# Optimization experiments

Measured on AMD Instinct MI355X. Metric: run time of the kernel, lower is better.

## Reference

```python
import jax, jax.numpy as jnp
import numpy as np

V, E, H, L, T, B = 50257, 1024, 16, 12, 128, 16
FF = 4 * E
STD = 0.02


def setup_inputs() -> dict:
    key = jax.random.key(0)
    ks = jax.random.split(key, 20)
    n = lambda k, shape: (jax.random.normal(k, shape, dtype=jnp.float32) * STD)
    inp = {
        'idx': jax.random.randint(ks[0], (B, T), 0, V, dtype=jnp.int64),
        'targets': jax.random.randint(ks[1], (B, T), 0, V, dtype=jnp.int64),
        'tok_emb': n(ks[2], (V, E)),
        'pos_emb': n(ks[3], (T, E)),
        'wq': n(ks[4], (L, E, E)),
        'wk': n(ks[5], (L, E, E)),
        'wv': n(ks[6], (L, E, E)),
        'w_proj': n(ks[7], (L, E, E)),
        'b_proj': jnp.zeros((L, E), jnp.float32),
        'ln1_g': jnp.ones((L, E), jnp.float32),
        'ln1_b': jnp.zeros((L, E), jnp.float32),
        'ln2_g': jnp.ones((L, E), jnp.float32),
        'ln2_b': jnp.zeros((L, E), jnp.float32),
        'w_fc1': n(ks[8], (L, E, FF)),
        'b_fc1': jnp.zeros((L, FF), jnp.float32),
        'w_fc2': n(ks[9], (L, FF, E)),
        'b_fc2': jnp.zeros((L, E), jnp.float32),
        'lnf_g': jnp.ones((E,), jnp.float32),
        'lnf_b': jnp.zeros((E,), jnp.float32),
        'w_head': n(ks[10], (E, V)),
        'b_head': jnp.zeros((V,), jnp.float32),
    }
    return inp


def _layernorm(x, g, b, eps=1e-5):
    m = x.mean(-1, keepdims=True)
    v = ((x - m) ** 2).mean(-1, keepdims=True)
    return (x - m) / jnp.sqrt(v + eps) * g + b


def _forward(idx, targets, tok_emb, pos_emb, wq, wk, wv, w_proj, b_proj,
             ln1_g, ln1_b, ln2_g, ln2_b, w_fc1, b_fc1, w_fc2, b_fc2,
             lnf_g, lnf_b, w_head, b_head):
    Bb, Tt = idx.shape
    x = tok_emb[idx] + pos_emb[:Tt]  # (B, T, E)
    causal = jnp.tril(jnp.ones((Tt, Tt), dtype=bool))
    scale = E ** (-0.5)  # NOTE: original scales by full n_embd, not head_size

    def block(x, p):
        (wq_l, wk_l, wv_l, wp_l, bp_l, g1, b1, g2, b2, wf1, bf1, wf2, bf2) = p
        h = _layernorm(x, g1, b1)
        q = (h @ wq_l).reshape(Bb, Tt, H, -1)
        k = (h @ wk_l).reshape(Bb, Tt, H, -1)
        v = (h @ wv_l).reshape(Bb, Tt, H, -1)
        sc = jnp.einsum('bthd,bshd->bhts', q, k) * scale
        sc = jnp.where(causal, sc, -jnp.inf)
        att = jax.nn.softmax(sc, axis=-1)
        o = jnp.einsum('bhts,bshd->bthd', att, v).reshape(Bb, Tt, E)
        x = x + o @ wp_l + bp_l
        h2 = _layernorm(x, g2, b2)
        x = x + jax.nn.relu(h2 @ wf1 + bf1) @ wf2 + bf2
        return x, None

    x, _ = jax.lax.scan(block, x, (wq, wk, wv, w_proj, b_proj, ln1_g, ln1_b,
                                   ln2_g, ln2_b, w_fc1, b_fc1, w_fc2, b_fc2))
    x = _layernorm(x, lnf_g, lnf_b)
    logits = x @ w_head + b_head  # (B, T, V)
    logp = jax.nn.log_softmax(logits, axis=-1)
    nll = -jnp.take_along_axis(logp.reshape(Bb * Tt, -1),
                               targets.reshape(-1, 1), axis=1)
    loss = nll.mean()
    return logits, loss


def reference(idx, targets, tok_emb, pos_emb, wq, wk, wv, w_proj, b_proj,
              ln1_g, ln1_b, ln2_g, ln2_b, w_fc1, b_fc1, w_fc2, b_fc2,
              lnf_g, lnf_b, w_head, b_head):
    return _forward(idx, targets, tok_emb, pos_emb, wq, wk, wv, w_proj, b_proj,
                    ln1_g, ln1_b, ln2_g, ln2_b, w_fc1, b_fc1, w_fc2, b_fc2,
                    lnf_g, lnf_b, w_head, b_head)
```

## Files before the change

### kernel.cpp

```cpp
#include <hip/hip_runtime.h>
#include <math.h>

typedef unsigned short u16;
typedef float f32x4 __attribute__((ext_vector_type(4)));
typedef short bf16x8 __attribute__((ext_vector_type(8)));
typedef unsigned short us4 __attribute__((ext_vector_type(4)));

#define DEVI __device__ __forceinline__

DEVI float bf2f(u16 u) { return __uint_as_float(((unsigned int)u) << 16); }
DEVI u16 f2bf(float f) {
    unsigned int u = __float_as_uint(f);
    u += 0x7fffu + ((u >> 16) & 1u);
    return (u16)(u >> 16);
}

__global__ __launch_bounds__(256) void k_embed(const int* __restrict__ idx,
                                               const float* __restrict__ te,
                                               const float* __restrict__ pe,
                                               float* __restrict__ x) {
    int m = blockIdx.x;
    int t = m & 127;
    int tok = idx[m];
    const f32x4* a = (const f32x4*)(te + (long)tok * 1024);
    const f32x4* p = (const f32x4*)(pe + (long)t * 1024);
    f32x4* o = (f32x4*)(x + (long)m * 1024);
    o[threadIdx.x] = a[threadIdx.x] + p[threadIdx.x];
}

__global__ __launch_bounds__(256) void k_ln(const float* __restrict__ x,
                                            const float* __restrict__ g,
                                            const float* __restrict__ b,
                                            u16* __restrict__ out) {
    __shared__ float red[8];
    int tid = threadIdx.x, lane = tid & 63, wid = tid >> 6;
    int r = blockIdx.x;
    f32x4 v = ((const f32x4*)(x + (long)r * 1024))[tid];
    float s = v.x + v.y + v.z + v.w;
#pragma unroll
    for (int o2 = 32; o2; o2 >>= 1) s += __shfl_xor(s, o2);
    if (lane == 0) red[wid] = s;
    __syncthreads();
    float mean = (red[0] + red[1] + red[2] + red[3]) * (1.0f / 1024.0f);
    f32x4 d; d.x = v.x - mean; d.y = v.y - mean; d.z = v.z - mean; d.w = v.w - mean;
    float sq = d.x * d.x + d.y * d.y + d.z * d.z + d.w * d.w;
#pragma unroll
    for (int o2 = 32; o2; o2 >>= 1) sq += __shfl_xor(sq, o2);
    if (lane == 0) red[4 + wid] = sq;
    __syncthreads();
    float rstd = rsqrtf((red[4] + red[5] + red[6] + red[7]) * (1.0f / 1024.0f) + 1e-5f);
    f32x4 gg = ((const f32x4*)g)[tid];
    f32x4 bb = ((const f32x4*)b)[tid];
    us4 o4;
    o4.x = f2bf(d.x * rstd * gg.x + bb.x);
    o4.y = f2bf(d.y * rstd * gg.y + bb.y);
    o4.z = f2bf(d.z * rstd * gg.z + bb.z);
    o4.w = f2bf(d.w * rstd * gg.w + bb.w);
    ((us4*)(out + (long)r * 1024))[tid] = o4;
}

DEVI void tr_tile(const float* __restrict__ in, u16* __restrict__ out,
                  int K, int N, int k0, int n0, int tid, float (*tile)[65]) {
    int trow = tid >> 4;
    int tcol = (tid & 15) * 4;
#pragma unroll
    for (int p = 0; p < 4; ++p) {
        int k = k0 + trow + p * 16;
        const float* src = in + (long)k * N + n0 + tcol;
#pragma unroll
        for (int j = 0; j < 4; ++j) {
            int n = n0 + tcol + j;
            tile[trow + p * 16][tcol + j] = (n < N) ? src[j] : 0.0f;
        }
    }
    __syncthreads();
#pragma unroll
    for (int p = 0; p < 4; ++p) {
        int n = n0 + trow + p * 16;
        if (n < N) {
            us4 o4;
#pragma unroll
            for (int j = 0; j < 4; ++j) o4[j] = f2bf(tile[tcol + j][trow + p * 16]);
            *(us4*)(out + (long)n * K + k0 + tcol) = o4;
        }
    }
}

__global__ __launch_bounds__(256) void k_tr_one(const float* __restrict__ in,
                                                u16* __restrict__ out, int K, int N) {
    __shared__ float tile[64][65];
    tr_tile(in, out, K, N, blockIdx.y * 64, blockIdx.x * 64, threadIdx.x, tile);
}

__global__ __launch_bounds__(256) void k_tr_layer(
    const float* __restrict__ wq, const float* __restrict__ wk,
    const float* __restrict__ wv, const float* __restrict__ wp,
    const float* __restrict__ f1, const float* __restrict__ f2,
    u16* __restrict__ oqkv, u16* __restrict__ oproj,
    u16* __restrict__ of1, u16* __restrict__ of2) {
    __shared__ float tile[64][65];
    int id = blockIdx.x;
    const float* in; u16* out; int K, N, txx, tyy;
    if (id < 1024) {
        int t = id >> 8, s2 = id & 255;
        txx = s2 & 15; tyy = s2 >> 4; K = 1024; N = 1024;
        in = (t == 0) ? wq : (t == 1) ? wk : (t == 2) ? wv : wp;
        out = (t == 3) ? oproj : oqkv + (long)t * 1024 * 1024;
    } else if (id < 2048) {
        int s2 = id - 1024;
        txx = s2 & 63; tyy = s2 >> 6; K = 1024; N = 4096; in = f1; out = of1;
    } else {
        int s2 = id - 2048;
        txx = s2 & 15; tyy = s2 >> 4; K = 4096; N = 1024; in = f2; out = of2;
    }
    tr_tile(in, out, K, N, tyy * 64, txx * 64, threadIdx.x, tile);
}

template <int ROWS>
DEVI void stage_tile(const u16* __restrict__ g, long row0, long rowmax, int ld,
                     int col0, char* lds, int tid) {
    constexpr int NCH = ROWS * 8;
#pragma unroll
    for (int p = 0; p < NCH / 256; ++p) {
        int c = tid + p * 256;
        int row = c >> 3;
        int gslot = c & 7;
        int gdata = gslot ^ (row & 7);
        long gr = row0 + row;
        if (gr > rowmax) gr = rowmax;
        const u16* src = g + gr * (long)ld + col0 + gdata * 8;
        char* dst = lds + ((long)((tid & 192) + p * 256)) * 16;
        __builtin_amdgcn_global_load_lds(
            (const __attribute__((address_space(1))) void*)src,
            (__attribute__((address_space(3))) void*)dst, 16, 0, 0);
    }
}

template <int ROWS>
DEVI void stage512(const u16* __restrict__ g, long row0, long rowmax, int ld,
                   int col0, char* lds, int tid) {
    constexpr int NP = ROWS * 8 / 512;
#pragma unroll
    for (int p = 0; p < NP; ++p) {
        int c = tid + p * 512;
        int row = c >> 3;
        int gslot = c & 7;
        int gdata = gslot ^ (row & 7);
        long gr = row0 + row;
        if (gr > rowmax) gr = rowmax;
        const u16* src = g + gr * (long)ld + col0 + gdata * 8;
        char* dst = lds + ((long)((tid & 448) + p * 512)) * 16;
        __builtin_amdgcn_global_load_lds(
            (const __attribute__((address_space(1))) void*)src,
            (__attribute__((address_space(3))) void*)dst, 16, 0, 0);
    }
}

template <int BN, bool OUT_BF16, bool RELU, bool HAS_BIAS, bool HAS_RES>
__global__ __launch_bounds__(256, 2) void k_gemm(
    const u16* __restrict__ A, const u16* __restrict__ Bt,
    const float* __restrict__ bias, const float* __restrict__ res,
    float* __restrict__ Cf, u16* __restrict__ Cb,
    int M, int N, int K, int ldc) {
    constexpr int NR = BN / 32;
    constexpr int ASZ = 128 * 64 * 2;
    constexpr int BSZ = BN * 64 * 2;
    __shared__ __align__(16) char lds[2 * (ASZ + BSZ)];
    int tid = threadIdx.x, lane = tid & 63, wid = tid >> 6;
    int l15 = lane & 15, l4 = lane >> 4;
    int wr = wid >> 1, wc = wid & 1;
    long m0 = (long)blockIdx.y * 128;
    long n0 = (long)blockIdx.x * BN;
    f32x4 acc[4][NR] = {};
    const int nk = K >> 6;

    stage_tile<128>(A, m0, (long)M - 1, K, 0, lds, tid);
    stage_tile<BN>(Bt, n0, (long)N - 1, K, 0, lds + ASZ, tid);
    int cur = 0;
    for (int kt = 0; kt < nk; ++kt) {
        __syncthreads();
        if (kt + 1 < nk) {
            char* nb = lds + (cur ^ 1) * (ASZ + BSZ);
            stage_tile<128>(A, m0, (long)M - 1, K, (kt + 1) << 6, nb, tid);
            stage_tile<BN>(Bt, n0, (long)N - 1, K, (kt + 1) << 6, nb + ASZ, tid);
        }
        const char* ab = lds + cur * (ASZ + BSZ);
        const char* bb = ab + ASZ;
#pragma unroll
        for (int kh = 0; kh < 2; ++kh) {
            bf16x8 af[4], bfv[NR];
#pragma unroll
            for (int mi = 0; mi < 4; ++mi) {
                int row = wr * 64 + mi * 16 + l15;
                int slot = (kh * 4 + l4) ^ (row & 7);
                af[mi] = *(const bf16x8*)(ab + (row * 8 + slot) * 16);
            }
#pragma unroll
            for (int ni = 0; ni < NR; ++ni) {
                int row = wc * (BN / 2) + ni * 16 + l15;
                int slot = (kh * 4 + l4) ^ (row & 7);
                bfv[ni] = *(const bf16x8*)(bb + (row * 8 + slot) * 16);
            }
#pragma unroll
            for (int mi = 0; mi < 4; ++mi)
#pragma unroll
                for (int ni = 0; ni < NR; ++ni)
                    acc[mi][ni] = __builtin_amdgcn_mfma_f32_16x16x32_bf16(
                        af[mi], bfv[ni], acc[mi][ni], 0, 0, 0);
        }
        cur ^= 1;
    }
#pragma unroll
    for (int ni = 0; ni < NR; ++ni) {
        long n = n0 + wc * (BN / 2) + ni * 16 + l15;
        if (n < N) {
            float bv = HAS_BIAS ? bias[n] : 0.0f;
#pragma unroll
            for (int mi = 0; mi < 4; ++mi) {
#pragma unroll
                for (int j = 0; j < 4; ++j) {
                    long m = m0 + wr * 64 + mi * 16 + l4 * 4 + j;
                    float v = acc[mi][ni][j] + bv;
                    if (HAS_RES) v += res[m * (long)ldc + n];
                    if (RELU) v = fmaxf(v, 0.0f);
                    if (OUT_BF16) Cb[m * (long)ldc + n] = f2bf(v);
                    else Cf[m * (long)ldc + n] = v;
                }
            }
        }
    }
}

__global__ __launch_bounds__(512, 1) void k_head256(
    const u16* __restrict__ A, const u16* __restrict__ Bt,
    const float* __restrict__ bias, float* __restrict__ Cf,
    float2* __restrict__ part, int M, int N, int K, int ldc) {
    constexpr int ASZ = 256 * 64 * 2;
    constexpr int BSZ = 128 * 64 * 2;
    __shared__ __align__(16) char lds[256 * 129 * 4];
    int tid = threadIdx.x, lane = tid & 63, wid = tid >> 6;
    int l15 = lane & 15, l4 = lane >> 4;
    int wr = wid >> 1, wc = wid & 1;
    int bn = blockIdx.x, bm = blockIdx.y;
    long m0 = (long)bm * 256, n0 = (long)bn * 128;
    f32x4 acc[4][4] = {};
    const int nk = K >> 6;

    stage512<256>(A, m0, (long)M - 1, K, 0, lds, tid);
    stage512<128>(Bt, n0, (long)N - 1, K, 0, lds + ASZ, tid);
    int cur = 0;
    for (int kt = 0; kt < nk; ++kt) {
        __syncthreads();
        if (kt + 1 < nk) {
            char* nb = lds + (cur ^ 1) * (ASZ + BSZ);
            stage512<256>(A, m0, (long)M - 1, K, (kt + 1) << 6, nb, tid);
            stage512<128>(Bt, n0, (long)N - 1, K, (kt + 1) << 6, nb + ASZ, tid);
        }
        const char* ab = lds + cur * (ASZ + BSZ);
        const char* bb = ab + ASZ;
#pragma unroll
        for (int kh = 0; kh < 2; ++kh) {
            bf16x8 af[4], bfv[4];
#pragma unroll
            for (int mi = 0; mi < 4; ++mi) {
                int row = wr * 64 + mi * 16 + l15;
                int slot = (kh * 4 + l4) ^ (row & 7);
                af[mi] = *(const bf16x8*)(ab + (row * 8 + slot) * 16);
            }
#pragma unroll
            for (int ni = 0; ni < 4; ++ni) {
                int row = wc * 64 + ni * 16 + l15;
                int slot = (kh * 4 + l4) ^ (row & 7);
                bfv[ni] = *(const bf16x8*)(bb + (row * 8 + slot) * 16);
            }
#pragma unroll
            for (int mi = 0; mi < 4; ++mi)
#pragma unroll
                for (int ni = 0; ni < 4; ++ni)
                    acc[mi][ni] = __builtin_amdgcn_mfma_f32_16x16x32_bf16(
                        af[mi], bfv[ni], acc[mi][ni], 0, 0, 0);
        }
        cur ^= 1;
    }
    const float BIG_NEG = -1e30f;
    float bvv[4];
#pragma unroll
    for (int ni = 0; ni < 4; ++ni) {
        long n = n0 + wc * 64 + ni * 16 + l15;
        bvv[ni] = (n < N) ? bias[n] : 0.0f;
    }
    __syncthreads();
    float* ldsF = (float*)lds;
#pragma unroll
    for (int mi = 0; mi < 4; ++mi)
#pragma unroll
        for (int ni = 0; ni < 4; ++ni)
#pragma unroll
            for (int j = 0; j < 4; ++j) {
                int row = wr * 64 + mi * 16 + l4 * 4 + j;
                int col = wc * 64 + ni * 16 + l15;
                long n = n0 + col;
                float v = acc[mi][ni][j] + bvv[ni];
                if (n >= N) v = BIG_NEG;
                ldsF[row * 129 + col] = v;
            }
    __syncthreads();
#pragma unroll 4
    for (int i = 0; i < 64; ++i) {
        int flat = tid + (i << 9);
        int row = flat >> 7, col = flat & 127;
        long n = n0 + col;
        if (n < N)
            __builtin_nontemporal_store(ldsF[row * 129 + col],
                                        &Cf[(m0 + row) * (long)ldc + n]);
    }
    {
        int r = tid >> 1, half = tid & 1;
        const float* rp = ldsF + r * 129 + half * 64;
        float mx = BIG_NEG;
#pragma unroll 8
        for (int c = 0; c < 64; ++c) mx = fmaxf(mx, rp[c]);
        float sm = 0.f;
#pragma unroll 8
        for (int c = 0; c < 64; ++c) sm += __expf(rp[c] - mx);
        float mo = __shfl_xor(mx, 1), so = __shfl_xor(sm, 1);
        float nm = fmaxf(mx, mo);
        float S = sm * __expf(mx - nm) + so * __expf(mo - nm);
        if (half == 0)
            part[(long)bn * M + m0 + r] = make_float2(nm, S);
    }
}

__global__ __launch_bounds__(256) void k_attn_mfma(const u16* __restrict__ qkv,
                                                   u16* __restrict__ o) {
    __shared__ __align__(16) u16 Ks[128 * 64];
    __shared__ __align__(16) u16 Vt[64 * 128];
    __shared__ __align__(16) u16 Ps[4][32 * 128];
    int tid = threadIdx.x, lane = tid & 63, w = tid >> 6;
    int l15 = lane & 15, l4 = lane >> 4;
    int b = blockIdx.x >> 4, h = blockIdx.x & 15;
    const u16* base = qkv + (long)b * 128 * 3072 + h * 64;

    stage_tile<128>(base + 1024, 0, 127, 3072, 0, (char*)Ks, tid);
    {
        const u16* vg = base + 2048;
#pragma unroll
        for (int p = 0; p < 4; ++p) {
            int s0 = (w * 4 + p) * 8;
            u16 tmp[8];
#pragma unroll
            for (int j = 0; j < 8; ++j) tmp[j] = vg[(long)(s0 + j) * 3072 + lane];
            int slot = (s0 >> 3) ^ (lane & 7);
            *(bf16x8*)((char*)Vt + lane * 256 + slot * 16) = *(bf16x8*)tmp;
        }
    }
    bf16x8 aq[2][2];
#pragma unroll
    for (int mj = 0; mj < 2; ++mj)
#pragma unroll
        for (int kk = 0; kk < 2; ++kk)
            aq[mj][kk] = *(const bf16x8*)(base + (long)(w * 32 + mj * 16 + l15) * 3072 + kk * 32 + l4 * 8);
    __syncthreads();

    f32x4 sacc[2][8] = {};
#pragma unroll
    for (int sj = 0; sj < 8; ++sj) {
        bf16x8 bk[2];
#pragma unroll
        for (int kk = 0; kk < 2; ++kk) {
            int row = sj * 16 + l15;
            int slot = (kk * 4 + l4) ^ (row & 7);
            bk[kk] = *(const bf16x8*)((char*)Ks + (row * 8 + slot) * 16);
        }
#pragma unroll
        for (int mj = 0; mj < 2; ++mj) {
            sacc[mj][sj] = __builtin_amdgcn_mfma_f32_16x16x32_bf16(aq[mj][0], bk[0], sacc[mj][sj], 0, 0, 0);
            sacc[mj][sj] = __builtin_amdgcn_mfma_f32_16x16x32_bf16(aq[mj][1], bk[1], sacc[mj][sj], 0, 0, 0);
        }
    }
    const float scale = 0.03125f;
#pragma unroll
    for (int mj = 0; mj < 2; ++mj) {
#pragma unroll
        for (int j = 0; j < 4; ++j) {
            int tq = w * 32 + mj * 16 + l4 * 4 + j;
            float mx = -INFINITY;
#pragma unroll
            for (int sj = 0; sj < 8; ++sj) {
                int s = sj * 16 + l15;
                float v = (s <= tq) ? sacc[mj][sj][j] * scale : -INFINITY;
                sacc[mj][sj][j] = v;
                mx = fmaxf(mx, v);
            }
#pragma unroll
            for (int ofs = 1; ofs < 16; ofs <<= 1) mx = fmaxf(mx, __shfl_xor(mx, ofs));
            float sm = 0.f;
#pragma unroll
            for (int sj = 0; sj < 8; ++sj) {
                float e = __expf(sacc[mj][sj][j] - mx);
                sacc[mj][sj][j] = e;
                sm += e;
            }
#pragma unroll
            for (int ofs = 1; ofs < 16; ofs <<= 1) sm += __shfl_xor(sm, ofs);
            float inv = 1.0f / sm;
            int m2 = mj * 16 + l4 * 4 + j;
            u16* prow = Ps[w] + m2 * 128;
#pragma unroll
            for (int sj = 0; sj < 8; ++sj) {
                int s = sj * 16 + l15;
                int slot = (s >> 3) ^ (m2 & 7);
                prow[slot * 8 + (s & 7)] = f2bf(sacc[mj][sj][j] * inv);
            }
        }
    }
    f32x4 oacc[2][4] = {};
#pragma unroll
    for (int kk = 0; kk < 4; ++kk) {
        bf16x8 pa[2], bv[4];
#pragma unroll
        for (int mj = 0; mj < 2; ++mj) {
            int m2 = mj * 16 + l15;
            int slot = (kk * 4 + l4) ^ (m2 & 7);
            pa[mj] = *(const bf16x8*)((char*)(Ps[w]) + m2 * 256 + slot * 16);
        }
#pragma unroll
        for (int nb = 0; nb < 4; ++nb) {
            int d = nb * 16 + l15;
            int slot = (kk * 4 + l4) ^ (d & 7);
            bv[nb] = *(const bf16x8*)((char*)Vt + d * 256 + slot * 16);
        }
#pragma unroll
        for (int mj = 0; mj < 2; ++mj)
#pragma unroll
            for (int nb = 0; nb < 4; ++nb)
                oacc[mj][nb] = __builtin_amdgcn_mfma_f32_16x16x32_bf16(pa[mj], bv[nb], oacc[mj][nb], 0, 0, 0);
    }
#pragma unroll
    for (int mj = 0; mj < 2; ++mj)
#pragma unroll
        for (int nb = 0; nb < 4; ++nb) {
            int d = nb * 16 + l15;
#pragma unroll
            for (int j = 0; j < 4; ++j) {
                int tq = w * 32 + mj * 16 + l4 * 4 + j;
                o[((long)b * 128 + tq) * 1024 + h * 64 + d] = f2bf(oacc[mj][nb][j]);
            }
        }
}

__global__ __launch_bounds__(64) void k_loss_rows2(const float2* __restrict__ part,
                                                   const float* __restrict__ logits,
                                                   const int* __restrict__ tgt,
                                                   float* __restrict__ rowloss, int ncb) {
    int r = blockIdx.x, lane = threadIdx.x;
    float M = -1e30f, S = 0.f;
    for (int cb = lane; cb < ncb; cb += 64) {
        float2 p = part[(long)cb * 2048 + r];
        float nm = fmaxf(M, p.x);
        S = S * __expf(M - nm) + p.y * __expf(p.x - nm);
        M = nm;
    }
#pragma unroll
    for (int ofs = 32; ofs; ofs >>= 1) {
        float M2 = __shfl_xor(M, ofs), S2 = __shfl_xor(S, ofs);
        float nm = fmaxf(M, M2);
        S = S * __expf(M - nm) + S2 * __expf(M2 - nm);
        M = nm;
    }
    if (lane == 0)
        rowloss[r] = (M + logf(S)) - logits[(long)r * 50257 + tgt[r]];
}

__global__ __launch_bounds__(256) void k_loss_reduce(const float* __restrict__ rowloss,
                                                     float* __restrict__ out) {
    __shared__ float red[4];
    int tid = threadIdx.x, lane = tid & 63, wid = tid >> 6;
    float s = 0.f;
    for (int i = tid; i < 2048; i += 256) s += rowloss[i];
#pragma unroll
    for (int ofs = 32; ofs; ofs >>= 1) s += __shfl_xor(s, ofs);
    if (lane == 0) red[wid] = s;
    __syncthreads();
    if (tid == 0) out[0] = (red[0] + red[1] + red[2] + red[3]) * (1.0f / 2048.0f);
}

extern "C" void kernel_launch(void* const* d_in, const int* in_sizes, int n_in,
                              void* d_out, int out_size, void* d_ws, size_t ws_size,
                              hipStream_t stream) {
    (void)in_sizes; (void)n_in; (void)out_size; (void)ws_size;
    const int*   idx     = (const int*)d_in[0];
    const int*   targets = (const int*)d_in[1];
    const float* tok_emb = (const float*)d_in[2];
    const float* pos_emb = (const float*)d_in[3];
    const float* wq      = (const float*)d_in[4];
    const float* wk      = (const float*)d_in[5];
    const float* wv      = (const float*)d_in[6];
    const float* w_proj  = (const float*)d_in[7];
    const float* b_proj  = (const float*)d_in[8];
    const float* ln1_g   = (const float*)d_in[9];
    const float* ln1_b   = (const float*)d_in[10];
    const float* ln2_g   = (const float*)d_in[11];
    const float* ln2_b   = (const float*)d_in[12];
    const float* w_fc1   = (const float*)d_in[13];
    const float* b_fc1   = (const float*)d_in[14];
    const float* w_fc2   = (const float*)d_in[15];
    const float* b_fc2   = (const float*)d_in[16];
    const float* lnf_g   = (const float*)d_in[17];
    const float* lnf_b   = (const float*)d_in[18];
    const float* w_head  = (const float*)d_in[19];
    const float* b_head  = (const float*)d_in[20];
    float* out = (float*)d_out;

    char* w = (char*)d_ws;
    auto alloc = [&](size_t bytes) {
        char* p = w;
        w += (bytes + 255) & ~(size_t)255;
        return p;
    };
    u16*    wT_qkv  = (u16*)alloc(3072L * 1024 * 2);
    u16*    wT_proj = (u16*)alloc(1024L * 1024 * 2);
    u16*    wT_f1   = (u16*)alloc(4096L * 1024 * 2);
    u16*    wT_f2   = (u16*)alloc(1024L * 4096 * 2);
    u16*    wT_head = (u16*)alloc(50257L * 1024 * 2);
    float*  x       = (float*)alloc(2048L * 1024 * 4);
    u16*    h_bf    = (u16*)alloc(2048L * 1024 * 2);
    u16*    qkvb    = (u16*)alloc(2048L * 3072 * 2);
    u16*    o_bf    = (u16*)alloc(2048L * 1024 * 2);
    u16*    ff_bf   = (u16*)alloc(2048L * 4096 * 2);
    float2* part    = (float2*)alloc(393L * 2048 * 8);
    float*  rowloss = (float*)alloc(2048L * 4);

    k_embed<<<2048, 256, 0, stream>>>(idx, tok_emb, pos_emb, x);
    k_tr_one<<<dim3(786, 16), 256, 0, stream>>>(w_head, wT_head, 1024, 50257);

    for (int l = 0; l < 12; ++l) {
        k_tr_layer<<<3072, 256, 0, stream>>>(
            wq + (long)l * 1048576, wk + (long)l * 1048576,
            wv + (long)l * 1048576, w_proj + (long)l * 1048576,
            w_fc1 + (long)l * 4194304, w_fc2 + (long)l * 4194304,
            wT_qkv, wT_proj, wT_f1, wT_f2);
        k_ln<<<2048, 256, 0, stream>>>(x, ln1_g + l * 1024, ln1_b + l * 1024, h_bf);
        k_gemm<128, true, false, false, false><<<dim3(24, 16), 256, 0, stream>>>(
            h_bf, wT_qkv, nullptr, nullptr, nullptr, qkvb, 2048, 3072, 1024, 3072);
        k_attn_mfma<<<256, 256, 0, stream>>>(qkvb, o_bf);
        k_gemm<64, false, false, true, true><<<dim3(16, 16), 256, 0, stream>>>(
            o_bf, wT_proj, b_proj + l * 1024, x, x, nullptr, 2048, 1024, 1024, 1024);
        k_ln<<<2048, 256, 0, stream>>>(x, ln2_g + l * 1024, ln2_b + l * 1024, h_bf);
        k_gemm<128, true, true, true, false><<<dim3(32, 16), 256, 0, stream>>>(
            h_bf, wT_f1, b_fc1 + l * 4096, nullptr, nullptr, ff_bf, 2048, 4096, 1024, 4096);
        k_gemm<64, false, false, true, true><<<dim3(16, 16), 256, 0, stream>>>(
            ff_bf, wT_f2, b_fc2 + l * 1024, x, x, nullptr, 2048, 1024, 4096, 1024);
    }
    k_ln<<<2048, 256, 0, stream>>>(x, lnf_g, lnf_b, h_bf);
    k_head256<<<dim3(393, 8), 512, 0, stream>>>(h_bf, wT_head, b_head, out, part,
                                                2048, 50257, 1024, 50257);
    k_loss_rows2<<<2048, 64, 0, stream>>>(part, out, targets, rowloss, 393);
    k_loss_reduce<<<1, 256, 0, stream>>>(rowloss, out + 102926336L);
}
```

Baseline: 2.059 ms.

## Triple-buffer LM head GEMM and split-K fc2 with residual folded into LayerNorm

The LM head GEMM moves from a double-buffered loop to a three-stage async LDS pipeline. It uses explicit vmcnt waits and raw barriers, and raises wave priority around the MFMA block. The fc2 GEMM is split into two K halves that write fp32 partial sums to a scratch buffer, which doubles the grid. A new combine+LayerNorm kernel then adds both partials, the bias and the residual, and applies the next LN1 or the final LN in one pass. This buys deeper load overlap and more parallelism, at the cost of extra partial-buffer traffic and more LDS in the head kernel.

Result: faster. 1.913 ms (-7.1%).

```diff
diff --git a/kernel.cpp b/kernel.cpp
--- a/kernel.cpp
+++ b/kernel.cpp
@@ -28,14 +28,8 @@
     o[threadIdx.x] = a[threadIdx.x] + p[threadIdx.x];
 }
 
-__global__ __launch_bounds__(256) void k_ln(const float* __restrict__ x,
-                                            const float* __restrict__ g,
-                                            const float* __restrict__ b,
-                                            u16* __restrict__ out) {
-    __shared__ float red[8];
-    int tid = threadIdx.x, lane = tid & 63, wid = tid >> 6;
-    int r = blockIdx.x;
-    f32x4 v = ((const f32x4*)(x + (long)r * 1024))[tid];
+DEVI void ln_body(f32x4 v, const float* g, const float* b, float* red,
+                  int tid, int lane, int wid, u16* outrow) {
     float s = v.x + v.y + v.z + v.w;
 #pragma unroll
     for (int o2 = 32; o2; o2 >>= 1) s += __shfl_xor(s, o2);
@@ -56,7 +50,37 @@
     o4.y = f2bf(d.y * rstd * gg.y + bb.y);
     o4.z = f2bf(d.z * rstd * gg.z + bb.z);
     o4.w = f2bf(d.w * rstd * gg.w + bb.w);
-    ((us4*)(out + (long)r * 1024))[tid] = o4;
+    ((us4*)outrow)[tid] = o4;
+}
+
+__global__ __launch_bounds__(256) void k_ln(const float* __restrict__ x,
+                                            const float* __restrict__ g,
+                                            const float* __restrict__ b,
+                                            u16* __restrict__ out) {
+    __shared__ float red[8];
+    int tid = threadIdx.x, lane = tid & 63, wid = tid >> 6;
+    int r = blockIdx.x;
+    f32x4 v = ((const f32x4*)(x + (long)r * 1024))[tid];
+    ln_body(v, g, b, red, tid, lane, wid, out + (long)r * 1024);
+}
+
+__global__ __launch_bounds__(256) void k_comb_ln(float* __restrict__ x,
+                                                 const float* __restrict__ p01,
+                                                 const float* __restrict__ bias,
+                                                 const float* __restrict__ g,
+                                                 const float* __restrict__ b,
+                                                 u16* __restrict__ out) {
+    __shared__ float red[8];
+    int tid = threadIdx.x, lane = tid & 63, wid = tid >> 6;
+    int r = blockIdx.x;
+    f32x4 v = ((const f32x4*)(x + (long)r * 1024))[tid];
+    f32x4 p0 = ((const f32x4*)(p01 + (long)r * 1024))[tid];
+    f32x4 p1 = ((const f32x4*)(p01 + 2048L * 1024 + (long)r * 1024))[tid];
+    f32x4 bv = ((const f32x4*)bias)[tid];
+    v.x += p0.x + p1.x + bv.x; v.y += p0.y + p1.y + bv.y;
+    v.z += p0.z + p1.z + bv.z; v.w += p0.w + p1.w + bv.w;
+    ((f32x4*)(x + (long)r * 1024))[tid] = v;
+    ln_body(v, g, b, red, tid, lane, wid, out + (long)r * 1024);
 }
 
 DEVI void tr_tile(const float* __restrict__ in, u16* __restrict__ out,
@@ -156,12 +180,12 @@
     }
 }
 
-template <int BN, bool OUT_BF16, bool RELU, bool HAS_BIAS, bool HAS_RES>
+template <int BN, bool OUT_BF16, bool RELU, bool HAS_BIAS, bool HAS_RES, bool SPLITK>
 __global__ __launch_bounds__(256, 2) void k_gemm(
     const u16* __restrict__ A, const u16* __restrict__ Bt,
     const float* __restrict__ bias, const float* __restrict__ res,
     float* __restrict__ Cf, u16* __restrict__ Cb,
-    int M, int N, int K, int ldc) {
+    int M, int N, int K, int ldk, int ldc) {
     constexpr int NR = BN / 32;
     constexpr int ASZ = 128 * 64 * 2;
     constexpr int BSZ = BN * 64 * 2;
@@ -169,20 +193,26 @@
     int tid = threadIdx.x, lane = tid & 63, wid = tid >> 6;
     int l15 = lane & 15, l4 = lane >> 4;
     int wr = wid >> 1, wc = wid & 1;
+    if constexpr (SPLITK) {
+        int h = blockIdx.z;
+        A += (long)h * K;
+        Bt += (long)h * K;
+        Cf += (long)h * M * (long)ldc;
+    }
     long m0 = (long)blockIdx.y * 128;
     long n0 = (long)blockIdx.x * BN;
     f32x4 acc[4][NR] = {};
     const int nk = K >> 6;
 
-    stage_tile<128>(A, m0, (long)M - 1, K, 0, lds, tid);
-    stage_tile<BN>(Bt, n0, (long)N - 1, K, 0, lds + ASZ, tid);
+    stage_tile<128>(A, m0, (long)M - 1, ldk, 0, lds, tid);
+    stage_tile<BN>(Bt, n0, (long)N - 1, ldk, 0, lds + ASZ, tid);
     int cur = 0;
     for (int kt = 0; kt < nk; ++kt) {
         __syncthreads();
         if (kt + 1 < nk) {
             char* nb = lds + (cur ^ 1) * (ASZ + BSZ);
-            stage_tile<128>(A, m0, (long)M - 1, K, (kt + 1) << 6, nb, tid);
-            stage_tile<BN>(Bt, n0, (long)N - 1, K, (kt + 1) << 6, nb + ASZ, tid);
+            stage_tile<128>(A, m0, (long)M - 1, ldk, (kt + 1) << 6, nb, tid);
+            stage_tile<BN>(Bt, n0, (long)N - 1, ldk, (kt + 1) << 6, nb + ASZ, tid);
         }
         const char* ab = lds + cur * (ASZ + BSZ);
         const char* bb = ab + ASZ;
@@ -237,7 +267,8 @@
     float2* __restrict__ part, int M, int N, int K, int ldc) {
     constexpr int ASZ = 256 * 64 * 2;
     constexpr int BSZ = 128 * 64 * 2;
-    __shared__ __align__(16) char lds[256 * 129 * 4];
+    constexpr int TSZ = ASZ + BSZ;
+    __shared__ __align__(16) char lds[3 * TSZ];
     int tid = threadIdx.x, lane = tid & 63, wid = tid >> 6;
     int l15 = lane & 15, l4 = lane >> 4;
     int wr = wid >> 1, wc = wid & 1;
@@ -246,17 +277,18 @@
     f32x4 acc[4][4] = {};
     const int nk = K >> 6;
 
-    stage512<256>(A, m0, (long)M - 1, K, 0, lds, tid);
-    stage512<128>(Bt, n0, (long)N - 1, K, 0, lds + ASZ, tid);
-    int cur = 0;
-    for (int kt = 0; kt < nk; ++kt) {
-        __syncthreads();
-        if (kt + 1 < nk) {
-            char* nb = lds + (cur ^ 1) * (ASZ + BSZ);
-            stage512<256>(A, m0, (long)M - 1, K, (kt + 1) << 6, nb, tid);
-            stage512<128>(Bt, n0, (long)N - 1, K, (kt + 1) << 6, nb + ASZ, tid);
-        }
-        const char* ab = lds + cur * (ASZ + BSZ);
+#pragma unroll
+    for (int t = 0; t < 3; ++t) {
+        char* buf = lds + t * TSZ;
+        stage512<256>(A, m0, (long)M - 1, K, t << 6, buf, tid);
+        stage512<128>(Bt, n0, (long)N - 1, K, t << 6, buf + ASZ, tid);
+    }
+    for (int t = 0; t < nk; ++t) {
+        if (t + 2 < nk)      asm volatile("s_waitcnt vmcnt(12)" ::: "memory");
+        else if (t + 1 < nk) asm volatile("s_waitcnt vmcnt(6)" ::: "memory");
+        else                 asm volatile("s_waitcnt vmcnt(0)" ::: "memory");
+        __builtin_amdgcn_s_barrier();
+        const char* ab = lds + (t % 3) * TSZ;
         const char* bb = ab + ASZ;
 #pragma unroll
         for (int kh = 0; kh < 2; ++kh) {
@@ -273,14 +305,21 @@
                 int slot = (kh * 4 + l4) ^ (row & 7);
                 bfv[ni] = *(const bf16x8*)(bb + (row * 8 + slot) * 16);
             }
+            __builtin_amdgcn_s_setprio(1);
 #pragma unroll
             for (int mi = 0; mi < 4; ++mi)
 #pragma unroll
                 for (int ni = 0; ni < 4; ++ni)
                     acc[mi][ni] = __builtin_amdgcn_mfma_f32_16x16x32_bf16(
                         af[mi], bfv[ni], acc[mi][ni], 0, 0, 0);
-        }
-        cur ^= 1;
+            __builtin_amdgcn_s_setprio(0);
+        }
+        __builtin_amdgcn_s_barrier();
+        if (t + 3 < nk) {
+            char* buf = lds + (t % 3) * TSZ;
+            stage512<256>(A, m0, (long)M - 1, K, (t + 3) << 6, buf, tid);
+            stage512<128>(Bt, n0, (long)N - 1, K, (t + 3) << 6, buf + ASZ, tid);
+        }
     }
     const float BIG_NEG = -1e30f;
     float bvv[4];
@@ -528,6 +567,7 @@
     u16*    qkvb    = (u16*)alloc(2048L * 3072 * 2);
     u16*    o_bf    = (u16*)alloc(2048L * 1024 * 2);
     u16*    ff_bf   = (u16*)alloc(2048L * 4096 * 2);
+    float*  p01     = (float*)alloc(2L * 2048 * 1024 * 4);
     float2* part    = (float2*)alloc(393L * 2048 * 8);
     float*  rowloss = (float*)alloc(2048L * 4);
 
@@ -540,19 +580,23 @@
             wv + (long)l * 1048576, w_proj + (long)l * 1048576,
             w_fc1 + (long)l * 4194304, w_fc2 + (long)l * 4194304,
             wT_qkv, wT_proj, wT_f1, wT_f2);
-        k_ln<<<2048, 256, 0, stream>>>(x, ln1_g + l * 1024, ln1_b + l * 1024, h_bf);
-        k_gemm<128, true, false, false, false><<<dim3(24, 16), 256, 0, stream>>>(
-            h_bf, wT_qkv, nullptr, nullptr, nullptr, qkvb, 2048, 3072, 1024, 3072);
+        if (l == 0)
+            k_ln<<<2048, 256, 0, stream>>>(x, ln1_g, ln1_b, h_bf);
+        else
+            k_comb_ln<<<2048, 256, 0, stream>>>(x, p01, b_fc2 + (l - 1) * 1024,
+                                                ln1_g + l * 1024, ln1_b + l * 1024, h_bf);
+        k_gemm<128, true, false, false, false, false><<<dim3(24, 16), 256, 0, stream>>>(
+            h_bf, wT_qkv, nullptr, nullptr, nullptr, qkvb, 2048, 3072, 1024, 1024, 3072);
         k_attn_mfma<<<256, 256, 0, stream>>>(qkvb, o_bf);
-        k_gemm<64, false, false, true, true><<<dim3(16, 16), 256, 0, stream>>>(
-            o_bf, wT_proj, b_proj + l * 1024, x, x, nullptr, 2048, 1024, 1024, 1024);
+        k_gemm<64, false, false, true, true, false><<<dim3(16, 16), 256, 0, stream>>>(
+            o_bf, wT_proj, b_proj + l * 1024, x, x, nullptr, 2048, 1024, 1024, 1024, 1024);
         k_ln<<<2048, 256, 0, stream>>>(x, ln2_g + l * 1024, ln2_b + l * 1024, h_bf);
-        k_gemm<128, true, true, true, false><<<dim3(32, 16), 256, 0, stream>>>(
-            h_bf, wT_f1, b_fc1 + l * 4096, nullptr, nullptr, ff_bf, 2048, 4096, 1024, 4096);
-        k_gemm<64, false, false, true, true><<<dim3(16, 16), 256, 0, stream>>>(
-            ff_bf, wT_f2, b_fc2 + l * 1024, x, x, nullptr, 2048, 1024, 4096, 1024);
-    }
-    k_ln<<<2048, 256, 0, stream>>>(x, lnf_g, lnf_b, h_bf);
+        k_gemm<128, true, true, true, false, false><<<dim3(32, 16), 256, 0, stream>>>(
+            h_bf, wT_f1, b_fc1 + l * 4096, nullptr, nullptr, ff_bf, 2048, 4096, 1024, 1024, 4096);
+        k_gemm<64, false, false, false, false, true><<<dim3(16, 16, 2), 256, 0, stream>>>(
+            ff_bf, wT_f2, nullptr, nullptr, p01, nullptr, 2048, 1024, 2048, 4096, 1024);
+    }
+    k_comb_ln<<<2048, 256, 0, stream>>>(x, p01, b_fc2 + 11 * 1024, lnf_g, lnf_b, h_bf);
     k_head256<<<dim3(393, 8), 512, 0, stream>>>(h_bf, wT_head, b_head, out, part,
                                                 2048, 50257, 1024, 50257);
     k_loss_rows2<<<2048, 64, 0, stream>>>(part, out, targets, rowloss, 393);
```
